# Optimization experiments

Measured on AMD Instinct MI355X. Metric: run time of the kernel, lower is better.

The kernel has to match this reference:

```python
import jax, jax.numpy as jnp
import numpy as np

H = 16      # heads
DH = 64     # dim_head
EPS = 1e-6
ROPE_BASE = 10000.0


def _rms_norm(t, w):
    # torch.nn.RMSNorm over last dim (inner_dim)
    var = jnp.mean(t * t, axis=-1, keepdims=True)
    return t * jax.lax.rsqrt(var + EPS) * w


def _rope(t):
    # t: (b, n, h, d) with d split as (d/2, 2) interleaved pairs
    b, n, h, d = t.shape
    theta = 1.0 / (ROPE_BASE ** (jnp.arange(0, d, 2, dtype=jnp.float32) / d))  # (d/2,)
    pos_theta = jnp.arange(n, dtype=jnp.float32)[:, None] * theta[None, :]     # (n, d/2)
    cos = jnp.cos(pos_theta)[None, :, None, :]  # (1, n, 1, d/2)
    sin = jnp.sin(pos_theta)[None, :, None, :]
    tp = t.reshape(b, n, h, d // 2, 2)
    x0, x1 = tp[..., 0], tp[..., 1]
    r0 = cos * x0 - sin * x1
    r1 = sin * x0 + cos * x1
    return jnp.stack([r0, r1], axis=-1).reshape(b, n, h, d)


def setup_inputs() -> dict:
    key = jax.random.key(0)
    ks = jax.random.split(key, 5)
    B, N, D = 2, 2048, 1024
    inner = H * DH
    scale = 1.0 / np.sqrt(D)
    return {
        "x": jax.random.normal(ks[0], (B, N, D), dtype=jnp.float32),
        "Wq": jax.random.normal(ks[1], (D, inner), dtype=jnp.float32) * scale,
        "Wkv": jax.random.normal(ks[2], (D, 2 * inner), dtype=jnp.float32) * scale,
        "norm_q_w": jnp.ones((inner,), dtype=jnp.float32),
        "norm_k_w": jnp.ones((inner,), dtype=jnp.float32),
        "Wo": jax.random.normal(ks[3], (inner, D), dtype=jnp.float32) * scale,
        "bo": jnp.zeros((D,), dtype=jnp.float32),
    }


def reference(x, Wq, Wkv, norm_q_w, norm_k_w, Wo, bo):
    B, N, D = x.shape
    q = x @ Wq                       # (b, n, inner)
    kv = x @ Wkv                     # (b, n, 2*inner)
    k, v = jnp.split(kv, 2, axis=-1)
    q = _rms_norm(q, norm_q_w)
    k = _rms_norm(k, norm_k_w)
    # (b, n, h, d)
    q = q.reshape(B, N, H, DH)
    k = k.reshape(B, N, H, DH)
    v = v.reshape(B, N, H, DH)
    q = _rope(q)
    k = _rope(k)
    # SDPA: softmax(q k^T / sqrt(d)) v, heads as batch dim
    scores = jnp.einsum("bnhd,bmhd->bhnm", q, k) / np.sqrt(DH)
    attn = jax.nn.softmax(scores, axis=-1)
    out = jnp.einsum("bhnm,bmhd->bnhd", attn, v).reshape(B, N, H * DH)
    return out @ Wo + bo
```

## Files before the change

kernel.cpp:

```cpp
#include <hip/hip_runtime.h>

typedef __bf16 bf16;
typedef _Float16 f16;
typedef __bf16 bf16x8 __attribute__((ext_vector_type(8)));
typedef _Float16 f16x4 __attribute__((ext_vector_type(4)));
typedef _Float16 f16x8 __attribute__((ext_vector_type(8)));
typedef float f32x4 __attribute__((ext_vector_type(4)));
typedef float f32x16 __attribute__((ext_vector_type(16)));

__device__ __forceinline__ void async16(const void* g, void* l) {
  __builtin_amdgcn_global_load_lds(
      (const __attribute__((address_space(1))) unsigned int*)g,
      (__attribute__((address_space(3))) unsigned int*)l, 16, 0, 0);
}

__device__ __forceinline__ unsigned cvtpk(float a, float b) {
  unsigned r;
  asm("v_cvt_pk_bf16_f32 %0, %1, %2" : "=v"(r) : "v"(a), "v"(b));
  return r;
}

__device__ __forceinline__ void swap32(unsigned& a, unsigned& b) {
  asm("v_permlane32_swap_b32 %0, %1" : "+v"(a), "+v"(b));
}

__global__ __launch_bounds__(256) void castx(const float* __restrict__ in,
                                             f16* __restrict__ out) {
  long i = ((long)blockIdx.x * 256 + threadIdx.x) * 4;
  f32x4 v = *(const f32x4*)(in + i);
  f16x4 o;
#pragma unroll
  for (int j = 0; j < 4; j++) o[j] = (f16)v[j];
  *(f16x4*)(out + i) = o;
}

__global__ __launch_bounds__(256) void tcast(const float* __restrict__ in,
                                             f16* __restrict__ out, int R, int C) {
  __shared__ float tile[32][33];
  int tx = threadIdx.x, ty = threadIdx.y;
  int c = blockIdx.x * 32 + tx;
#pragma unroll
  for (int i = 0; i < 4; i++) {
    int r = blockIdx.y * 32 + ty + i * 8;
    tile[ty + i * 8][tx] = in[(long)r * C + c];
  }
  __syncthreads();
  int c2 = blockIdx.y * 32 + tx;
#pragma unroll
  for (int i = 0; i < 4; i++) {
    int r2 = blockIdx.x * 32 + ty + i * 8;
    out[(long)r2 * R + c2] = (f16)tile[tx][ty + i * 8];
  }
}

__global__ __launch_bounds__(256) void vtrans(const f16* __restrict__ src,
                                              bf16* __restrict__ vt) {
  __shared__ f16 tile[32][33];
  int tx = threadIdx.x, ty = threadIdx.y;
  int n0 = blockIdx.x * 32, d0 = blockIdx.y * 32, bh = blockIdx.z;
  int b = bh >> 4, h = bh & 15;
#pragma unroll
  for (int i = 0; i < 4; i++) {
    int n = n0 + ty + i * 8;
    tile[ty + i * 8][tx] = src[(long)(b * 2048 + n) * 3072 + h * 64 + d0 + tx];
  }
  __syncthreads();
#pragma unroll
  for (int i = 0; i < 4; i++) {
    int d = d0 + ty + i * 8;
    vt[((long)(bh * 64 + d)) * 2048 + n0 + tx] = (bf16)(float)tile[tx][ty + i * 8];
  }
}

template <int MODE>
__global__ __launch_bounds__(512) void gemm_f16(const f16* __restrict__ A_g,
                                                const f16* __restrict__ B_g,
                                                float* __restrict__ p0,
                                                float* __restrict__ p1,
                                                f16* __restrict__ outh,
                                                int M, int N, int K) {
  __shared__ __align__(16) f16 AL[2][4096], BL[2][4096];
  int t = threadIdx.x, lane = t & 63, w = t >> 6;
  int wm = w >> 1, wn = w & 1;
  int m0 = blockIdx.y * 128, n0 = blockIdx.x * 128;
  int fm = lane & 15, fq = lane >> 4;
  int kseg = K / gridDim.z;
  int kstart = blockIdx.z * kseg;
  int nk = kseg / 32;

  const f16* ap = A_g + (long)(m0 + w * 16 + fm) * K + kstart + fq * 8;
  const f16* bp = B_g + (long)(n0 + w * 16 + fm) * K + kstart + fq * 8;

  f32x4 acc[2][4];
#pragma unroll
  for (int i = 0; i < 2; i++)
#pragma unroll
    for (int j = 0; j < 4; j++) acc[i][j] = f32x4{0.f, 0.f, 0.f, 0.f};

  async16(ap, &AL[0][w * 512]);
  async16(bp, &BL[0][w * 512]);

  for (int it = 0; it < nk; it++) {
    int cur = it & 1;
    __syncthreads();
    if (it < nk - 1) {
      int ko = (it + 1) * 32;
      async16(ap + ko, &AL[cur ^ 1][w * 512]);
      async16(bp + ko, &BL[cur ^ 1][w * 512]);
    }
    f16x8 a[2], bfr[4];
#pragma unroll
    for (int i = 0; i < 2; i++)
      a[i] = *(const f16x8*)&AL[cur][(wm * 2 + i) * 512 + lane * 8];
#pragma unroll
    for (int j = 0; j < 4; j++)
      bfr[j] = *(const f16x8*)&BL[cur][(wn * 4 + j) * 512 + lane * 8];
#pragma unroll
    for (int i = 0; i < 2; i++)
#pragma unroll
      for (int j = 0; j < 4; j++)
        acc[i][j] = __builtin_amdgcn_mfma_f32_16x16x32_f16(a[i], bfr[j], acc[i][j], 0, 0, 0);
  }

  float* dst = blockIdx.z ? p1 : p0;
#pragma unroll
  for (int i = 0; i < 2; i++)
#pragma unroll
    for (int j = 0; j < 4; j++) {
      int c = n0 + (wn * 4 + j) * 16 + fm;
#pragma unroll
      for (int e = 0; e < 4; e++) {
        int r = m0 + (wm * 2 + i) * 16 + fq * 4 + e;
        if (MODE == 0)
          dst[(long)r * N + c] = acc[i][j][e];
        else
          outh[(long)r * N + c] = (f16)acc[i][j][e];
      }
    }
}

__global__ __launch_bounds__(256) void addbias(const float* __restrict__ p0,
                                               const float* __restrict__ p1,
                                               const float* __restrict__ bias,
                                               float* __restrict__ out) {
  long i = ((long)blockIdx.x * 256 + threadIdx.x) * 4;
  f32x4 a = *(const f32x4*)(p0 + i);
  f32x4 b = *(const f32x4*)(p1 + i);
  f32x4 c = *(const f32x4*)(bias + (i & 1023));
  *(f32x4*)(out + i) = a + b + c;
}

__global__ __launch_bounds__(256) void normrope(const f16* __restrict__ src,
                                                const float* __restrict__ wqn,
                                                const float* __restrict__ wkn,
                                                f16* __restrict__ qf,
                                                f16* __restrict__ kf) {
  int row = blockIdx.x, which = blockIdx.y;
  const f16* sp = src + (long)row * 3072 + which * 1024;
  const float* w = which ? wkn : wqn;
  f16* oh = which ? kf : qf;
  float scale = which ? 1.0f : 0.125f;
  int t = threadIdx.x;
  int j0 = t * 4;

  f16x4 xh = *(const f16x4*)(sp + j0);
  float xv[4];
#pragma unroll
  for (int j = 0; j < 4; j++) xv[j] = (float)xh[j];
  float ss = xv[0] * xv[0] + xv[1] * xv[1] + xv[2] * xv[2] + xv[3] * xv[3];
#pragma unroll
  for (int off = 32; off > 0; off >>= 1) ss += __shfl_down(ss, off);
  __shared__ float red[4];
  if ((t & 63) == 0) red[t >> 6] = ss;
  __syncthreads();
  float total = red[0] + red[1] + red[2] + red[3];
  float nsc = rsqrtf(total * (1.0f / 1024.0f) + 1e-6f) * scale;

  int n = row & 2047;
  f16x4 o;
#pragma unroll
  for (int pp = 0; pp < 2; pp++) {
    int j = j0 + 2 * pp;
    int ii = (j & 63) >> 1;
    float theta = __expf((float)ii * (-9.210340371976184f / 32.0f));
    float ang = (float)n * theta;
    float sn, cs;
    __sincosf(ang, &sn, &cs);
    float a0 = xv[2 * pp] * nsc * w[j];
    float a1 = xv[2 * pp + 1] * nsc * w[j + 1];
    o[2 * pp] = (f16)(cs * a0 - sn * a1);
    o[2 * pp + 1] = (f16)(sn * a0 + cs * a1);
  }
  *(f16x4*)(oh + (long)row * 1024 + j0) = o;
}

__global__ __launch_bounds__(256) void attn_mfma(const f16* __restrict__ qf,
                                                 const f16* __restrict__ kf,
                                                 const bf16* __restrict__ vt,
                                                 f16* __restrict__ af) {
  __shared__ __align__(16) f16 KhL[2][4096];
  __shared__ __align__(16) bf16 VtL[2][4096];

  int t = threadIdx.x;
  int lane = t & 63, w = t >> 6;
  int lo5 = lane & 31, hi = lane >> 5;
  int b = blockIdx.z, h = blockIdx.y, q0 = blockIdx.x * 128;

  const f16* qb = qf + ((long)(b * 2048 + q0 + w * 32 + lo5)) * 1024 + h * 64 + hi * 8;
  f16x8 qfr[4];
#pragma unroll
  for (int ks = 0; ks < 4; ks++) qfr[ks] = *(const f16x8*)(qb + ks * 16);

  int r8 = lane >> 3;
  int ch = (lane & 7) ^ r8;
  const char* kgb = (const char*)(kf + ((long)(b * 2048)) * 1024 + h * 64);
  const char* vgb = (const char*)(vt + ((long)((b * 16 + h) * 64)) * 2048);

  int koff[4];
#pragma unroll
  for (int ks = 0; ks < 4; ks++)
    koff[ks] = lo5 * 128 + ((ks * 32 + hi * 16) ^ ((lane & 7) << 4));

  f32x16 Ot[2];
#pragma unroll
  for (int i = 0; i < 16; i++) {
    Ot[0][i] = 0.f;
    Ot[1][i] = 0.f;
  }
  float l_ = 0.f;

#define STAGE(buf, kb)                                                        \
  {                                                                           \
    _Pragma("unroll") for (int uu = 0; uu < 2; uu++) {                        \
      int u = w * 2 + uu;                                                     \
      async16(kgb + ((long)((kb) * 64 + u * 8 + r8)) * 2048 + ch * 16,        \
              (char*)KhL[buf] + u * 1024);                                    \
      async16(vgb + ((long)(u * 8 + r8)) * 4096 + (long)(kb) * 128 + ch * 16, \
              (char*)VtL[buf] + u * 1024);                                    \
    }                                                                         \
  }

  STAGE(0, 0);

  for (int kb = 0; kb < 32; kb++) {
    int cur = kb & 1;
    __syncthreads();
    if (kb < 31) STAGE(cur ^ 1, kb + 1);

    const char* kbase = (const char*)KhL[cur];
    const char* vbase = (const char*)VtL[cur];

    f32x16 s0, s1;
#pragma unroll
    for (int i = 0; i < 16; i++) {
      s0[i] = 0.f;
      s1[i] = 0.f;
    }
#pragma unroll
    for (int ks = 0; ks < 4; ks++) {
      f16x8 k0 = *(const f16x8*)(kbase + koff[ks]);
      f16x8 k1 = *(const f16x8*)(kbase + 4096 + koff[ks]);
      s0 = __builtin_amdgcn_mfma_f32_32x32x16_f16(k0, qfr[ks], s0, 0, 0, 0);
      s1 = __builtin_amdgcn_mfma_f32_32x32x16_f16(k1, qfr[ks], s1, 0, 0, 0);
    }

    union PF {
      unsigned u[4];
      bf16x8 v;
    } pf[4];
#pragma unroll
    for (int nt = 0; nt < 2; nt++) {
      f32x16 s = nt ? s1 : s0;
      float pv[16];
#pragma unroll
      for (int r = 0; r < 16; r++) {
        pv[r] = __expf(s[r]);
        l_ += pv[r];
      }
#pragma unroll
      for (int g = 0; g < 2; g++) {
        unsigned c01 = cvtpk(pv[g * 8 + 0], pv[g * 8 + 1]);
        unsigned c23 = cvtpk(pv[g * 8 + 2], pv[g * 8 + 3]);
        unsigned c45 = cvtpk(pv[g * 8 + 4], pv[g * 8 + 5]);
        unsigned c67 = cvtpk(pv[g * 8 + 6], pv[g * 8 + 7]);
        swap32(c01, c45);
        swap32(c23, c67);
        pf[nt * 2 + g].u[0] = c01;
        pf[nt * 2 + g].u[1] = c23;
        pf[nt * 2 + g].u[2] = c45;
        pf[nt * 2 + g].u[3] = c67;
      }
    }

#pragma unroll
    for (int ks = 0; ks < 4; ks++) {
      bf16x8 v0 = *(const bf16x8*)(vbase + koff[ks]);
      bf16x8 v1 = *(const bf16x8*)(vbase + 4096 + koff[ks]);
      Ot[0] = __builtin_amdgcn_mfma_f32_32x32x16_bf16(v0, pf[ks].v, Ot[0], 0, 0, 0);
      Ot[1] = __builtin_amdgcn_mfma_f32_32x32x16_bf16(v1, pf[ks].v, Ot[1], 0, 0, 0);
    }
  }
#undef STAGE

  l_ += __shfl_xor(l_, 32);
  float inv = 1.0f / l_;

  f16* op = af + ((long)(b * 2048 + q0 + w * 32 + lo5)) * 1024 + h * 64;
#pragma unroll
  for (int dt = 0; dt < 2; dt++)
#pragma unroll
    for (int g4 = 0; g4 < 4; g4++) {
      f16x4 o4;
#pragma unroll
      for (int e = 0; e < 4; e++) o4[e] = (f16)(Ot[dt][g4 * 4 + e] * inv);
      *(f16x4*)(op + dt * 32 + g4 * 8 + hi * 4) = o4;
    }
}

extern "C" void kernel_launch(void* const* d_in, const int* in_sizes, int n_in,
                              void* d_out, int out_size, void* d_ws, size_t ws_size,
                              hipStream_t stream) {
  const float* x = (const float*)d_in[0];
  const float* Wq = (const float*)d_in[1];
  const float* Wkv = (const float*)d_in[2];
  const float* nqw = (const float*)d_in[3];
  const float* nkw = (const float*)d_in[4];
  const float* Wo = (const float*)d_in[5];
  const float* bo = (const float*)d_in[6];
  float* out = (float*)d_out;

  char* ws = (char*)d_ws;
  const long MB = 1l << 20;
  f16* xf     = (f16*)(ws);
  f16* Wqkv_t = (f16*)(ws + 8 * MB);
  f16* qkv_f  = (f16*)(ws + 14 * MB);
  f16* qfb    = (f16*)(ws + 38 * MB);
  f16* kfb    = (f16*)(ws + 46 * MB);
  bf16* vtb   = (bf16*)(ws + 54 * MB);
  f16* afb    = (f16*)(ws);
  f16* Wo_t   = (f16*)(ws + 8 * MB);
  float* p0   = (float*)(ws + 14 * MB);
  float* p1   = (float*)(ws + 30 * MB);

  dim3 tb(32, 8);
  castx<<<4096, 256, 0, stream>>>(x, xf);
  tcast<<<dim3(32, 32), tb, 0, stream>>>(Wq, Wqkv_t, 1024, 1024);
  tcast<<<dim3(64, 32), tb, 0, stream>>>(Wkv, Wqkv_t + 1024l * 1024, 1024, 2048);

  gemm_f16<1><<<dim3(24, 32), 512, 0, stream>>>(xf, Wqkv_t, nullptr, nullptr,
                                                qkv_f, 4096, 3072, 1024);

  normrope<<<dim3(4096, 2), 256, 0, stream>>>(qkv_f, nqw, nkw, qfb, kfb);

  vtrans<<<dim3(64, 2, 32), tb, 0, stream>>>(qkv_f + 2048, vtb);

  attn_mfma<<<dim3(16, 16, 2), 256, 0, stream>>>(qfb, kfb, vtb, afb);

  tcast<<<dim3(32, 32), tb, 0, stream>>>(Wo, Wo_t, 1024, 1024);

  gemm_f16<0><<<dim3(8, 32, 2), 512, 0, stream>>>(afb, Wo_t, p0, p1, nullptr,
                                                  4096, 1024, 1024);

  addbias<<<4096, 256, 0, stream>>>(p0, p1, bo, out);
}
```

Before: 239.1 us.

## Split attention over the key dimension and merge partial results in a combine kernel

```diff
diff --git a/kernel.cpp b/kernel.cpp
--- a/kernel.cpp
+++ b/kernel.cpp
@@ -197,14 +197,17 @@
 __global__ __launch_bounds__(256) void attn_mfma(const f16* __restrict__ qf,
                                                  const f16* __restrict__ kf,
                                                  const bf16* __restrict__ vt,
-                                                 f16* __restrict__ af) {
+                                                 f16* __restrict__ pO,
+                                                 float* __restrict__ pl) {
   __shared__ __align__(16) f16 KhL[2][4096];
   __shared__ __align__(16) bf16 VtL[2][4096];
 
   int t = threadIdx.x;
   int lane = t & 63, w = t >> 6;
   int lo5 = lane & 31, hi = lane >> 5;
-  int b = blockIdx.z, h = blockIdx.y, q0 = blockIdx.x * 128;
+  int z = blockIdx.z;
+  int b = z >> 1, ksp = z & 1;
+  int h = blockIdx.y, q0 = blockIdx.x * 128;
 
   const f16* qb = qf + ((long)(b * 2048 + q0 + w * 32 + lo5)) * 1024 + h * 64 + hi * 8;
   f16x8 qfr[4];
@@ -228,6 +231,8 @@
     Ot[1][i] = 0.f;
   }
   float l_ = 0.f;
+
+  int kb0 = ksp * 16;
 
 #define STAGE(buf, kb)                                                        \
   {                                                                           \
@@ -240,12 +245,12 @@
     }                                                                         \
   }
 
-  STAGE(0, 0);
-
-  for (int kb = 0; kb < 32; kb++) {
-    int cur = kb & 1;
+  STAGE(0, kb0);
+
+  for (int it = 0; it < 16; it++) {
+    int cur = it & 1;
     __syncthreads();
-    if (kb < 31) STAGE(cur ^ 1, kb + 1);
+    if (it < 15) STAGE(cur ^ 1, kb0 + it + 1);
 
     const char* kbase = (const char*)KhL[cur];
     const char* vbase = (const char*)VtL[cur];
@@ -305,7 +310,8 @@
   l_ += __shfl_xor(l_, 32);
   float inv = 1.0f / l_;
 
-  f16* op = af + ((long)(b * 2048 + q0 + w * 32 + lo5)) * 1024 + h * 64;
+  long rowi = ((long)((ksp * 2 + b) * 16 + h)) * 2048 + q0 + w * 32 + lo5;
+  f16* op = pO + rowi * 64;
 #pragma unroll
   for (int dt = 0; dt < 2; dt++)
 #pragma unroll
@@ -315,6 +321,26 @@
       for (int e = 0; e < 4; e++) o4[e] = (f16)(Ot[dt][g4 * 4 + e] * inv);
       *(f16x4*)(op + dt * 32 + g4 * 8 + hi * 4) = o4;
     }
+  if (hi == 0) pl[rowi] = l_;
+}
+
+__global__ __launch_bounds__(256) void attn_combine(const f16* __restrict__ pO,
+                                                    const float* __restrict__ pl,
+                                                    f16* __restrict__ af) {
+  int dg = threadIdx.x & 15;
+  int qi = threadIdx.x >> 4;
+  int q = blockIdx.x * 16 + qi;
+  int h = blockIdx.y, b = blockIdx.z;
+  long r0 = ((long)(b * 16 + h)) * 2048 + q;
+  long r1 = ((long)((2 + b) * 16 + h)) * 2048 + q;
+  float l0 = pl[r0], l1 = pl[r1];
+  float w0 = l0 / (l0 + l1), w1 = 1.0f - w0;
+  f16x4 a = *(const f16x4*)(pO + r0 * 64 + dg * 4);
+  f16x4 c = *(const f16x4*)(pO + r1 * 64 + dg * 4);
+  f16x4 o;
+#pragma unroll
+  for (int e = 0; e < 4; e++) o[e] = (f16)((float)a[e] * w0 + (float)c[e] * w1);
+  *(f16x4*)(af + ((long)(b * 2048 + q)) * 1024 + h * 64 + dg * 4) = o;
 }
 
 extern "C" void kernel_launch(void* const* d_in, const int* in_sizes, int n_in,
@@ -337,6 +363,8 @@
   f16* qfb    = (f16*)(ws + 38 * MB);
   f16* kfb    = (f16*)(ws + 46 * MB);
   bf16* vtb   = (bf16*)(ws + 54 * MB);
+  f16* pOb    = (f16*)(ws + 14 * MB);
+  float* plb  = (float*)(ws + 30 * MB);
   f16* afb    = (f16*)(ws);
   f16* Wo_t   = (f16*)(ws + 8 * MB);
   float* p0   = (float*)(ws + 14 * MB);
@@ -354,7 +382,9 @@
 
   vtrans<<<dim3(64, 2, 32), tb, 0, stream>>>(qkv_f + 2048, vtb);
 
-  attn_mfma<<<dim3(16, 16, 2), 256, 0, stream>>>(qfb, kfb, vtb, afb);
+  attn_mfma<<<dim3(16, 16, 4), 256, 0, stream>>>(qfb, kfb, vtb, pOb, plb);
+
+  attn_combine<<<dim3(128, 16, 2), 256, 0, stream>>>(pOb, plb, afb);
 
   tcast<<<dim3(32, 32), tb, 0, stream>>>(Wo, Wo_t, 1024, 1024);
 
```

New measurement: 250.7 us. 1.05x slower.
